# Kernel tuning notes

Measured on AMD Instinct MI355X. Metric: run time of the kernel, lower is better.

The kernel has to match this reference:

```python
import jax, jax.numpy as jnp
import numpy as np

N_NODES = 12288
N_EDGES = 393216  # N_NODES * avg_degree 32
IN_DIM, H1, H2 = 1433, 32, 16


def setup_inputs() -> dict:
    key = jax.random.key(0)
    ks = jax.random.split(key, 7)

    def glorot(k, fan_in, fan_out):
        r = np.sqrt(6.0 / (fan_in + fan_out)).astype(np.float32)
        return jax.random.uniform(k, (fan_in, fan_out), jnp.float32, -r, r)

    return {
        "X": jax.random.normal(ks[0], (N_NODES, IN_DIM), jnp.float32),
        "W1": glorot(ks[1], IN_DIM, H1),
        "W2": glorot(ks[2], H1, H1),
        "W3": glorot(ks[3], H1, H2),
        "edge_val": jax.random.uniform(ks[4], (N_EDGES,), jnp.float32),
        "edge_row": jax.random.randint(ks[5], (N_EDGES,), 0, N_NODES, jnp.int32),
        "edge_col": jax.random.randint(ks[6], (N_EDGES,), 0, N_NODES, jnp.int32),
    }


def reference(X, W1, W2, W3, edge_val, edge_row, edge_col):
    n = X.shape[0]

    def spmm(x):
        # sparse adj (COO) @ x : gather source rows, scale, scatter-add to dest
        return jax.ops.segment_sum(edge_val[:, None] * x[edge_col], edge_row, num_segments=n)

    h = jax.nn.relu(spmm(X @ W1))       # [N, 32]
    h = jax.nn.relu(spmm(h @ W2))       # [N, 32]
    Z = spmm(h @ W3)                    # [N, 16] (identity activation)
    A_pred = jax.nn.sigmoid(Z @ Z.T)    # [N, N] dot-product decode
    return (A_pred, Z)
```

## Files before the change

kernel.cpp:

```cpp
#include <hip/hip_runtime.h>


constexpr int NN = 12288;
constexpr int NE = 393216;
constexpr int KD = 1433;
constexpr int CAP = 96;

typedef float f32x4 __attribute__((ext_vector_type(4)));
typedef float f32x4u __attribute__((ext_vector_type(4), aligned(4)));
typedef float f32x16 __attribute__((ext_vector_type(16)));
typedef short shortx8 __attribute__((ext_vector_type(8)));

__device__ __forceinline__ unsigned short f2bf(float v) {
    unsigned int b = __float_as_uint(v);
    return (unsigned short)((b + 0x7FFFu + ((b >> 16) & 1u)) >> 16);
}

constexpr int KC = 256;
constexpr int NCH = 6;
constexpr int XST = KC + 8;
constexpr int G1B = (NN / 64) * NCH;

__global__ __launch_bounds__(256) void k_scatter_gemm1(const int* __restrict__ er,
                                                       const int* __restrict__ ec,
                                                       const float* __restrict__ ev,
                                                       int* __restrict__ cnt,
                                                       uint2* __restrict__ ebuf,
                                                       const float* __restrict__ X,
                                                       const float* __restrict__ W,
                                                       float* __restrict__ out) {
    if (blockIdx.x >= G1B) {
        int e = (blockIdx.x - G1B) * 256 + threadIdx.x;
        int r = er[e];
        int p = atomicAdd(&cnt[r], 1);
        if (p < CAP) ebuf[(size_t)r * CAP + p] = make_uint2((unsigned)ec[e], __float_as_uint(ev[e]));
        return;
    }
    __shared__ unsigned short wt[32 * XST];

    int rgB   = blockIdx.x / NCH;
    int chunk = blockIdx.x % NCH;
    int r0 = rgB * 64;
    int k0 = chunk * KC;
    int kt = min(KC, KD - k0);
    int nm = (kt + 15) >> 4;
    int t = threadIdx.x;

    int wtot = nm * 16 * 32;
    for (int e = t; e < wtot; e += 256) {
        int k = e >> 5, c = e & 31;
        float v = (k < kt) ? W[(size_t)(k0 + k) * 32 + c] : 0.f;
        wt[c * XST + k] = f2bf(v);
    }
    __syncthreads();

    int w = t >> 6, l = t & 63;
    int rg = w >> 1;
    int lr = l & 31, lh = l >> 5;
    int row = r0 + rg * 32 + lr;
    const float* xr = X + (size_t)row * KD + k0 + lh * 8;
    const unsigned short* wbase = wt + lr * XST + lh * 8;
    f32x16 acc = {0.f};
    for (int m = (w & 1); m < nm; m += 2) {
        int kk = m * 16 + lh * 8;
        float xv[8];
        if (kk + 8 <= kt) {
            f32x4u v0 = *(const f32x4u*)(xr + m * 16);
            f32x4u v1 = *(const f32x4u*)(xr + m * 16 + 4);
#pragma unroll
            for (int j = 0; j < 4; ++j) { xv[j] = v0[j]; xv[4 + j] = v1[j]; }
        } else {
#pragma unroll
            for (int j = 0; j < 8; ++j) xv[j] = (kk + j < kt) ? xr[m * 16 + j] : 0.f;
        }
        shortx8 a;
#pragma unroll
        for (int j = 0; j < 8; ++j) a[j] = (short)f2bf(xv[j]);
        shortx8 b = *(const shortx8*)(wbase + m * 16);
        acc = __builtin_amdgcn_mfma_f32_32x32x16_bf16(a, b, acc, 0, 0, 0);
    }
#pragma unroll
    for (int q = 0; q < 16; ++q) {
        int rf = (q & 3) + 8 * (q >> 2) + 4 * lh;
        atomicAdd(&out[(size_t)(r0 + rg * 32 + rf) * 32 + lr], acc[q]);
    }
}

__global__ __launch_bounds__(256) void spmm_gemm32(const float* __restrict__ in,
                                                   const float* __restrict__ Wm,
                                                   float* __restrict__ out,
                                                   const int* __restrict__ cnt,
                                                   const uint2* __restrict__ ebuf) {
    int tid = blockIdx.x * 256 + threadIdx.x;
    int r = tid >> 6;
    int lane = threadIdx.x & 63;
    int c = lane & 31, half = lane >> 5;
    float wcol[32];
#pragma unroll
    for (int k = 0; k < 32; ++k) wcol[k] = Wm[k * 32 + c];
    int deg = min(cnt[r], CAP);
    int mid = (deg >> 1) & ~1;
    int lo = half ? mid : 0;
    int hi = half ? deg : mid;
    const uint2* eb2 = ebuf + (size_t)r * CAP;
    const uint4* eb4 = (const uint4*)eb2;
    float acc = 0.f;
    int i = lo;
#pragma unroll 2
    for (; i + 4 <= hi; i += 4) {
        uint4 e01 = eb4[i >> 1], e23 = eb4[(i >> 1) + 1];
        acc += __uint_as_float(e01.y) * in[(size_t)e01.x * 32 + c];
        acc += __uint_as_float(e01.w) * in[(size_t)e01.z * 32 + c];
        acc += __uint_as_float(e23.y) * in[(size_t)e23.x * 32 + c];
        acc += __uint_as_float(e23.w) * in[(size_t)e23.z * 32 + c];
    }
    for (; i < hi; ++i) {
        uint2 e = eb2[i];
        acc += __uint_as_float(e.y) * in[(size_t)e.x * 32 + c];
    }
    float h = fmaxf(acc + __shfl_xor(acc, 32), 0.f);
    float o = 0.f;
#pragma unroll
    for (int k = 0; k < 32; ++k)
        o += __shfl(h, (lane & 32) + k) * wcol[k];
    if (half == 0) out[(size_t)r * 32 + c] = o;
}

__global__ __launch_bounds__(256) void spmm32(const float* __restrict__ in,
                                              float* __restrict__ out,
                                              const int* __restrict__ cnt,
                                              const uint2* __restrict__ ebuf) {
    int tid = blockIdx.x * 256 + threadIdx.x;
    int r = tid >> 6;
    int lane = threadIdx.x & 63;
    int c = lane & 31, half = lane >> 5;
    int deg = min(cnt[r], CAP);
    int mid = (deg >> 1) & ~1;
    int lo = half ? mid : 0;
    int hi = half ? deg : mid;
    const uint2* eb2 = ebuf + (size_t)r * CAP;
    const uint4* eb4 = (const uint4*)eb2;
    float acc = 0.f;
    int i = lo;
#pragma unroll 2
    for (; i + 4 <= hi; i += 4) {
        uint4 e01 = eb4[i >> 1], e23 = eb4[(i >> 1) + 1];
        acc += __uint_as_float(e01.y) * in[(size_t)e01.x * 32 + c];
        acc += __uint_as_float(e01.w) * in[(size_t)e01.z * 32 + c];
        acc += __uint_as_float(e23.y) * in[(size_t)e23.x * 32 + c];
        acc += __uint_as_float(e23.w) * in[(size_t)e23.z * 32 + c];
    }
    for (; i < hi; ++i) {
        uint2 e = eb2[i];
        acc += __uint_as_float(e.y) * in[(size_t)e.x * 32 + c];
    }
    float s = acc + __shfl_xor(acc, 32);
    if (half == 0) out[(size_t)r * 32 + c] = s;
}

__global__ __launch_bounds__(256) void spmm_w3(const float* __restrict__ in,
                                               const float* __restrict__ Wm,
                                               float* __restrict__ Z,
                                               unsigned short* __restrict__ zb,
                                               const int* __restrict__ cnt,
                                               const uint2* __restrict__ ebuf) {
    int tid = blockIdx.x * 256 + threadIdx.x;
    int r = tid >> 6;
    int lane = threadIdx.x & 63;
    int c = lane & 31, half = lane >> 5;
    int co = c & 15;
    float wcol[32];
#pragma unroll
    for (int k = 0; k < 32; ++k) wcol[k] = Wm[k * 16 + co];
    int deg = min(cnt[r], CAP);
    int mid = (deg >> 1) & ~1;
    int lo = half ? mid : 0;
    int hi = half ? deg : mid;
    const uint2* eb2 = ebuf + (size_t)r * CAP;
    const uint4* eb4 = (const uint4*)eb2;
    float acc = 0.f;
    int i = lo;
#pragma unroll 2
    for (; i + 4 <= hi; i += 4) {
        uint4 e01 = eb4[i >> 1], e23 = eb4[(i >> 1) + 1];
        acc += __uint_as_float(e01.y) * fmaxf(in[(size_t)e01.x * 32 + c], 0.f);
        acc += __uint_as_float(e01.w) * fmaxf(in[(size_t)e01.z * 32 + c], 0.f);
        acc += __uint_as_float(e23.y) * fmaxf(in[(size_t)e23.x * 32 + c], 0.f);
        acc += __uint_as_float(e23.w) * fmaxf(in[(size_t)e23.z * 32 + c], 0.f);
    }
    for (; i < hi; ++i) {
        uint2 e = eb2[i];
        acc += __uint_as_float(e.y) * fmaxf(in[(size_t)e.x * 32 + c], 0.f);
    }
    float g = acc + __shfl_xor(acc, 32);
    float o = 0.f;
#pragma unroll
    for (int k = 0; k < 32; ++k)
        o += __shfl(g, (lane & 32) + k) * wcol[k];
    if (half == 0 && c < 16) {
        Z[(size_t)r * 16 + co] = o;
        zb[(size_t)r * 16 + co] = f2bf(o);
    }
}

__global__ __launch_bounds__(256) void decode_mfma(const unsigned short* __restrict__ Zb,
                                                   float* __restrict__ A) {
    __shared__ float ts[64][260];
    int id = blockIdx.x;
    int f = (id & 7) * (9216 / 8) + (id >> 3);
    int bi = f / 48, bj = f % 48;
    int w = threadIdx.x >> 6;
    int l = threadIdx.x & 63;
    int R = bi * 64;
    int C = bj * 256 + w * 64;
    int lr = l & 31, lh = l >> 5;

    shortx8 a0 = *(const shortx8*)(Zb + ((size_t)(R + lr) << 4) + lh * 8);
    shortx8 a1 = *(const shortx8*)(Zb + ((size_t)(R + 32 + lr) << 4) + lh * 8);
    shortx8 b0 = *(const shortx8*)(Zb + ((size_t)(C + lr) << 4) + lh * 8);
    shortx8 b1 = *(const shortx8*)(Zb + ((size_t)(C + 32 + lr) << 4) + lh * 8);

    f32x16 acc00 = {0.f}, acc01 = {0.f}, acc10 = {0.f}, acc11 = {0.f};
    acc00 = __builtin_amdgcn_mfma_f32_32x32x16_bf16(a0, b0, acc00, 0, 0, 0);
    acc01 = __builtin_amdgcn_mfma_f32_32x32x16_bf16(a0, b1, acc01, 0, 0, 0);
    acc10 = __builtin_amdgcn_mfma_f32_32x32x16_bf16(a1, b0, acc10, 0, 0, 0);
    acc11 = __builtin_amdgcn_mfma_f32_32x32x16_bf16(a1, b1, acc11, 0, 0, 0);

    int cw = w * 64;
#pragma unroll
    for (int q = 0; q < 16; ++q) {
        int rf = (q & 3) + 8 * (q >> 2) + 4 * lh;
        ts[rf][cw + lr]           = __fdividef(1.0f, 1.0f + __expf(-acc00[q]));
        ts[rf][cw + 32 + lr]      = __fdividef(1.0f, 1.0f + __expf(-acc01[q]));
        ts[32 + rf][cw + lr]      = __fdividef(1.0f, 1.0f + __expf(-acc10[q]));
        ts[32 + rf][cw + 32 + lr] = __fdividef(1.0f, 1.0f + __expf(-acc11[q]));
    }
    __syncthreads();

    int C0 = bj * 256;
#pragma unroll
    for (int i = 0; i < 16; ++i) {
        int flat = i * 256 + threadIdx.x;
        int row = flat >> 6;
        int c4 = (flat & 63) << 2;
        f32x4 v = *(const f32x4*)&ts[row][c4];
        __builtin_nontemporal_store(v, (f32x4*)&A[(size_t)(R + row) * NN + C0 + c4]);
    }
}

extern "C" void kernel_launch(void* const* d_in, const int* in_sizes, int n_in,
                              void* d_out, int out_size, void* d_ws, size_t ws_size,
                              hipStream_t stream) {
    const float* X  = (const float*)d_in[0];
    const float* W1 = (const float*)d_in[1];
    const float* W2 = (const float*)d_in[2];
    const float* W3 = (const float*)d_in[3];
    const float* ev = (const float*)d_in[4];
    const int*   er = (const int*)d_in[5];
    const int*   ec = (const int*)d_in[6];

    float* A = (float*)d_out;
    float* Z = A + (size_t)NN * NN;

    int*   cnt = (int*)d_ws;
    float* t1 = (float*)(cnt + NN);
    float* t2 = t1 + (size_t)NN * 32;
    float* t3 = t2 + (size_t)NN * 32;
    unsigned short* Zb = (unsigned short*)t1;

    uint2* ebuf = (uint2*)(A + (size_t)140000000);

    (void)hipMemsetAsync(cnt, 0, NN * sizeof(int) + (size_t)NN * 32 * sizeof(float), stream);

    k_scatter_gemm1<<<G1B + NE / 256, 256, 0, stream>>>(er, ec, ev, cnt, ebuf, X, W1, t1);

    spmm_gemm32<<<NN * 64 / 256, 256, 0, stream>>>(t1, W2, t2, cnt, ebuf);
    spmm32<<<NN * 64 / 256, 256, 0, stream>>>(t2, t3, cnt, ebuf);
    spmm_w3<<<NN * 64 / 256, 256, 0, stream>>>(t3, W3, Z, Zb, cnt, ebuf);

    decode_mfma<<<192 * 48, 256, 0, stream>>>(Zb, A);
}
```

Baseline: 199.3 us.

## Stage X tile through shared memory as bf16 with coalesced loads, halve K chunk

The first GEMM now loads a 64x128 tile of X cooperatively with contiguous float4 reads, converts it to bf16 once and stores it in LDS. The MFMA loop then reads both operands from LDS instead of per-lane strided global loads with inline conversion. The K chunk shrinks from 256 to 128, doubling the chunk count so the LDS tile fits and more blocks run. The trade-off is twice as many atomic partial-sum writes to the output plus a sync barrier with no overlap of load and compute.

```diff
diff --git a/kernel.cpp b/kernel.cpp
--- a/kernel.cpp
+++ b/kernel.cpp
@@ -10,15 +10,16 @@
 typedef float f32x4u __attribute__((ext_vector_type(4), aligned(4)));
 typedef float f32x16 __attribute__((ext_vector_type(16)));
 typedef short shortx8 __attribute__((ext_vector_type(8)));
+typedef unsigned short u16x4 __attribute__((ext_vector_type(4)));
 
 __device__ __forceinline__ unsigned short f2bf(float v) {
     unsigned int b = __float_as_uint(v);
     return (unsigned short)((b + 0x7FFFu + ((b >> 16) & 1u)) >> 16);
 }
 
-constexpr int KC = 256;
-constexpr int NCH = 6;
-constexpr int XST = KC + 8;
+constexpr int KC = 128;
+constexpr int NCH = 12;
+constexpr int XST = 136;
 constexpr int G1B = (NN / 64) * NCH;
 
 __global__ __launch_bounds__(256) void k_scatter_gemm1(const int* __restrict__ er,
@@ -36,6 +37,7 @@
         if (p < CAP) ebuf[(size_t)r * CAP + p] = make_uint2((unsigned)ec[e], __float_as_uint(ev[e]));
         return;
     }
+    __shared__ unsigned short xs[64 * XST];
     __shared__ unsigned short wt[32 * XST];
 
     int rgB   = blockIdx.x / NCH;
@@ -52,30 +54,34 @@
         float v = (k < kt) ? W[(size_t)(k0 + k) * 32 + c] : 0.f;
         wt[c * XST + k] = f2bf(v);
     }
+    if (kt == KC) {
+#pragma unroll
+        for (int it = 0; it < 8; ++it) {
+            int idx = it * 1024 + t * 4;
+            int row = idx >> 7, k = idx & 127;
+            f32x4u v = *(const f32x4u*)(X + (size_t)(r0 + row) * KD + k0 + k);
+            u16x4 p;
+            p[0] = f2bf(v[0]); p[1] = f2bf(v[1]); p[2] = f2bf(v[2]); p[3] = f2bf(v[3]);
+            *(u16x4*)(xs + row * XST + k) = p;
+        }
+    } else {
+        for (int e = t; e < 64 * 32; e += 256) {
+            int row = e >> 5, k = e & 31;
+            float v = (k < kt) ? X[(size_t)(r0 + row) * KD + k0 + k] : 0.f;
+            xs[row * XST + k] = f2bf(v);
+        }
+    }
     __syncthreads();
 
     int w = t >> 6, l = t & 63;
     int rg = w >> 1;
+    int par = w & 1;
     int lr = l & 31, lh = l >> 5;
-    int row = r0 + rg * 32 + lr;
-    const float* xr = X + (size_t)row * KD + k0 + lh * 8;
+    const unsigned short* xbase = xs + (rg * 32 + lr) * XST + lh * 8;
     const unsigned short* wbase = wt + lr * XST + lh * 8;
     f32x16 acc = {0.f};
-    for (int m = (w & 1); m < nm; m += 2) {
-        int kk = m * 16 + lh * 8;
-        float xv[8];
-        if (kk + 8 <= kt) {
-            f32x4u v0 = *(const f32x4u*)(xr + m * 16);
-            f32x4u v1 = *(const f32x4u*)(xr + m * 16 + 4);
-#pragma unroll
-            for (int j = 0; j < 4; ++j) { xv[j] = v0[j]; xv[4 + j] = v1[j]; }
-        } else {
-#pragma unroll
-            for (int j = 0; j < 8; ++j) xv[j] = (kk + j < kt) ? xr[m * 16 + j] : 0.f;
-        }
-        shortx8 a;
-#pragma unroll
-        for (int j = 0; j < 8; ++j) a[j] = (short)f2bf(xv[j]);
+    for (int m = par; m < nm; m += 2) {
+        shortx8 a = *(const shortx8*)(xbase + m * 16);
         shortx8 b = *(const shortx8*)(wbase + m * 16);
         acc = __builtin_amdgcn_mfma_f32_32x32x16_bf16(a, b, acc, 0, 0, 0);
     }
```

Result: slower. 209.0 us (+4.9%).
